# Performance work log

Measured on AMD Instinct MI355X. Metric: run time of the kernel, lower is better.

The kernel has to match this reference:

```python
import jax, jax.numpy as jnp
import numpy as np

B, S, D, H, L = 2, 4096, 768, 12, 2
DH = D // H
W = 256            # one-sided sliding window (longformer-base attention_window=512)
VOCAB = 50265
SEP_ID = 2
N_SEPS = 63
G = N_SEPS + 1     # global tokens: <s> at pos 0 + all </s> separators
FF = 4 * D
C = 7
NEG = -1e9


def layer_norm(x, s, b, eps=1e-5):
    m = x.mean(-1, keepdims=True)
    v = ((x - m) ** 2).mean(-1, keepdims=True)
    return (x - m) * jax.lax.rsqrt(v + eps) * s + b


def setup_inputs():
    key = jax.random.key(0)
    keys = iter(jax.random.split(key, 64))
    def nrm(shape, sd=0.02):
        return jax.random.normal(next(keys), shape, jnp.float32) * sd
    input_ids = jax.random.randint(next(keys), (B, S), 5, VOCAB, dtype=jnp.int32)
    input_ids = input_ids.at[:, 0].set(0)  # <s>
    sep_pos = (jnp.arange(N_SEPS) + 1) * (S // (N_SEPS + 1))  # 64,128,...,4032
    input_ids = input_ids.at[:, sep_pos].set(SEP_ID)
    return dict(
        emb_tok=nrm((VOCAB, D)), emb_pos=nrm((S, D)),
        ln_e_s=jnp.ones((D,)), ln_e_b=jnp.zeros((D,)),
        Wq=nrm((L, D, D)), bq=jnp.zeros((L, D)),
        Wk=nrm((L, D, D)), bk=jnp.zeros((L, D)),
        Wv=nrm((L, D, D)), bv=jnp.zeros((L, D)),
        Wqg=nrm((L, D, D)), bqg=jnp.zeros((L, D)),
        Wkg=nrm((L, D, D)), bkg=jnp.zeros((L, D)),
        Wvg=nrm((L, D, D)), bvg=jnp.zeros((L, D)),
        Wo=nrm((L, D, D)), bo=jnp.zeros((L, D)),
        ln1_s=jnp.ones((L, D)), ln1_b=jnp.zeros((L, D)),
        Wf1=nrm((L, D, FF)), bf1=jnp.zeros((L, FF)),
        Wf2=nrm((L, FF, D)), bf2=jnp.zeros((L, D)),
        ln2_s=jnp.ones((L, D)), ln2_b=jnp.zeros((L, D)),
        Wc=nrm((D, C)), bc=jnp.zeros((C,)),
        input_ids=input_ids,
        attention_mask=jnp.ones((B, S), jnp.int32),
        left_overlap=2, right_overlap=2,
    )


def _forward(emb_tok, emb_pos, ln_e_s, ln_e_b, Wq, bq, Wk, bk, Wv, bv,
             Wqg, bqg, Wkg, bkg, Wvg, bvg, Wo, bo, ln1_s, ln1_b,
             Wf1, bf1, Wf2, bf2, ln2_s, ln2_b, Wc, bc,
             input_ids, attention_mask, left_overlap, right_overlap):
    pos = jnp.arange(S)
    # global attention mask: first token + every </s> token (as in the torch forward)
    g_mask = (input_ids == SEP_ID) | (pos[None, :] == 0)                         # [B,S]
    idx_g = jax.vmap(lambda m: jnp.nonzero(m, size=G, fill_value=0)[0])(g_mask)  # [B,G]
    am = attention_mask.astype(jnp.float32)
    key_local_ok = am * (1.0 - g_mask.astype(jnp.float32))  # globals excluded from windowed keys
    nb = S // W
    band_idx = jnp.arange(nb)[:, None] * W + jnp.arange(3 * W)[None, :]  # [nb,3W] into W-padded seq
    rel = jnp.arange(3 * W)[None, :] - W - jnp.arange(W)[:, None]        # key_pos - query_pos
    band_ok = (jnp.abs(rel) <= W)[None, None, None]                       # [1,1,1,W,3W]
    kv_ok = jnp.pad(key_local_ok, ((0, 0), (W, W)))[:, band_idx] > 0      # [B,nb,3W]
    mask = band_ok & kv_ok[:, None, :, None, :]                           # [B,1,nb,W,3W]
    scale = float(DH) ** -0.5
    bix = jnp.arange(B)[:, None]

    x = emb_tok[input_ids] + emb_pos[None]
    x = layer_norm(x, ln_e_s, ln_e_b)
    for l in range(L):
        q = (x @ Wq[l] + bq[l]).reshape(B, S, H, DH)
        k = (x @ Wk[l] + bk[l]).reshape(B, S, H, DH)
        v = (x @ Wv[l] + bv[l]).reshape(B, S, H, DH)
        kb = jnp.pad(k, ((0, 0), (W, W), (0, 0), (0, 0)))[:, band_idx]    # [B,nb,3W,H,DH]
        vb = jnp.pad(v, ((0, 0), (W, W), (0, 0), (0, 0)))[:, band_idx]
        s_band = jnp.einsum('bnqhd,bnkhd->bhnqk', q.reshape(B, nb, W, H, DH), kb) * scale
        s_band = jnp.where(mask, s_band, NEG)
        kg = jnp.take_along_axis(k, idx_g[:, :, None, None], axis=1)      # [B,G,H,DH]
        vg = jnp.take_along_axis(v, idx_g[:, :, None, None], axis=1)
        s_glob = jnp.einsum('bqhd,bghd->bhqg', q, kg) * scale
        probs = jax.nn.softmax(
            jnp.concatenate([s_band.reshape(B, H, S, 3 * W), s_glob], axis=-1), axis=-1)
        out = (jnp.einsum('bhnqk,bnkhd->bnqhd',
                          probs[..., :3 * W].reshape(B, H, nb, W, 3 * W), vb).reshape(B, S, H, DH)
               + jnp.einsum('bhqg,bghd->bqhd', probs[..., 3 * W:], vg)).reshape(B, S, D)
        # global query rows: full attention over all tokens with dedicated global projections
        xg = jnp.take_along_axis(x, idx_g[:, :, None], axis=1)            # [B,G,D]
        qg = (xg @ Wqg[l] + bqg[l]).reshape(B, G, H, DH)
        kga = (x @ Wkg[l] + bkg[l]).reshape(B, S, H, DH)
        vga = (x @ Wvg[l] + bvg[l]).reshape(B, S, H, DH)
        sg = jnp.where(am[:, None, None, :] > 0,
                       jnp.einsum('bghd,bshd->bhgs', qg, kga) * scale, NEG)
        og = jnp.einsum('bhgs,bshd->bghd', jax.nn.softmax(sg, axis=-1), vga).reshape(B, G, D)
        out = out.at[bix, idx_g].set(og)
        x = layer_norm(x + out @ Wo[l] + bo[l], ln1_s[l], ln1_b[l])
        x = layer_norm(x + jax.nn.gelu(x @ Wf1[l] + bf1[l]) @ Wf2[l] + bf2[l], ln2_s[l], ln2_b[l])
    # classification head (eval-mode dropout = identity). Faithful to the torch code,
    # which gathers hidden states at token POSITION j for j in [left, n_seps - right).
    core = x[:, left_overlap:N_SEPS - right_overlap, :]                    # [B, n_core, D]
    return (core @ Wc + bc).reshape(-1, C)


def reference(emb_tok, emb_pos, ln_e_s, ln_e_b, Wq, bq, Wk, bk, Wv, bv,
              Wqg, bqg, Wkg, bkg, Wvg, bvg, Wo, bo, ln1_s, ln1_b,
              Wf1, bf1, Wf2, bf2, ln2_s, ln2_b, Wc, bc,
              input_ids, attention_mask, left_overlap, right_overlap):
    return _forward(emb_tok, emb_pos, ln_e_s, ln_e_b, Wq, bq, Wk, bk, Wv, bv,
                    Wqg, bqg, Wkg, bkg, Wvg, bvg, Wo, bo, ln1_s, ln1_b,
                    Wf1, bf1, Wf2, bf2, ln2_s, ln2_b, Wc, bc,
                    input_ids, attention_mask, left_overlap, right_overlap)
```

## Files before the change

kernel.cpp:

```cpp
#include <hip/hip_runtime.h>
#include <hip/hip_bf16.h>
#include <stdint.h>

#define B_ 2
#define S_ 4096
#define D_ 768
#define H_ 12
#define DH_ 64
#define L_ 2
#define W_ 256
#define G_ 64
#define FF_ 3072
#define C_ 7
#define SEP_ 2
#define NEG_ (-1000000000.0f)
#define NC_ 16

typedef __attribute__((ext_vector_type(8))) short short8;
typedef __attribute__((ext_vector_type(4))) float f32x4;

__device__ __forceinline__ float bfu2f(unsigned short u) {
    return __uint_as_float(((unsigned int)u) << 16);
}
__device__ __forceinline__ unsigned short f2bfu(float f) {
// ... 172 lines not shown
    int slice = bz;
    int kper = K / gridDim.z;
    int kbeg = slice * kper;
    GEMM256_CORE(A, Wt, K, kbeg, kper);
    float bj[4];
#pragma unroll
    for (int nj = 0; nj < 4; nj++)
        bj[nj] = (slice == 0) ? bias[n0 + (wc << 6) + nj * 16 + l16] : 0.f;
    float* outp = (slice == 0) ? Cf : Cf2;
#pragma unroll
    for (int mi = 0; mi < 8; mi++)
#pragma unroll
        for (int nj = 0; nj < 4; nj++) {
            int col = n0 + (wc << 6) + nj * 16 + l16;
#pragma unroll
            for (int rr = 0; rr < 4; rr++) {
                int row = m0 + (wr << 7) + mi * 16 + quad * 4 + rr;
                float v = acc[mi][nj][rr] + bj[nj];
                if (act) v = gelu_tanh(v);
                if (outp) outp[(size_t)row * N + col] = v;
                else      Cb[(size_t)row * N + col] = f2bfu(v);
            }
        }
}

struct P5 {
    const unsigned short* Wt[5];
    const float* Wf[5];
    const float* bias[5];
    unsigned short* out[5];
};
__global__ __launch_bounds__(512, 1) void k_qkv5_256(
    const unsigned short* __restrict__ A, P5 p) {
    int bx = blockIdx.x, by = blockIdx.y, bz = blockIdx.z;
    xcd_remap(bx, by, bz);
    const unsigned short* __restrict__ Wt = p.Wt[bz];
    const float* __restrict__ bias = p.bias[bz];
    unsigned short* __restrict__ Cb = p.out[bz];
    const int K = D_;
    int m0 = by << 8, n0 = bx << 8;
    GEMM256_CORE(A, Wt, K, 0, K);
    float bj[4];
#pragma unroll
    for (int nj = 0; nj < 4; nj++) bj[nj] = bias[n0 + (wc << 6) + nj * 16 + l16];
#pragma unroll
    for (int mi = 0; mi < 8; mi++)
#pragma unroll
        for (int nj = 0; nj < 4; nj++) {
            int col = n0 + (wc << 6) + nj * 16 + l16;
#pragma unroll
            for (int rr = 0; rr < 4; rr++) {
                int row = m0 + (wr << 7) + mi * 16 + quad * 4 + rr;
                float v = acc[mi][nj][rr] + bj[nj];
                size_t adr = ((((size_t)(row >> 12)) * H_ + (col >> 6)) * S_ +
                              (row & (S_ - 1))) * DH_ + (col & 63);
                Cb[adr] = f2bfu(v);
            }
        }
}

#define GEMM_COMPUTE(Ab, Bb)                                                             \
    {                                                                                    \
        short8 af[4], bf[4];                                                             \
        _Pragma("unroll")                                                                \
        for (int i_ = 0; i_ < 4; i_++)                                                   \
            af[i_] = *(const short8*)&(Ab)[(wm + i_ * 16 + l16) * 32 + quad * 8];        \
        _Pragma("unroll")                                                                \
        for (int j_ = 0; j_ < 4; j_++)                                                   \
            bf[j_] = *(const short8*)&(Bb)[(wn + j_ * 16 + l16) * 32 + quad * 8];        \
        _Pragma("unroll")                                                                \
        for (int i_ = 0; i_ < 4; i_++)                                                   \
            _Pragma("unroll")                                                            \
            for (int j_ = 0; j_ < 4; j_++)                                               \
                acc[i_][j_] = __builtin_amdgcn_mfma_f32_16x16x32_bf16(af[i_], bf[j_],    \
                                                                      acc[i_][j_], 0, 0, 0); \
    }

#define WAIT_VM0_BARRIER()                                   \
    {                                                        \
        asm volatile("s_waitcnt vmcnt(0)" ::: "memory");     \
        __builtin_amdgcn_s_barrier();                        \
    }

__global__ __launch_bounds__(256) void k_wtrans(
    const float* __restrict__ src, unsigned short* __restrict__ dst,
    int K, int N, size_t dstStride) {
    int l = blockIdx.z;
    src += (size_t)l * K * N;
    dst += (size_t)l * dstStride;
    __shared__ unsigned short tile[32][36];
    int t = threadIdx.x;
    int r = t >> 3, c4 = (t & 7) << 2;
    int k0 = blockIdx.y << 5, n0 = blockIdx.x << 5;
    float4 v = *(const float4*)(src + (size_t)(k0 + r) * N + n0 + c4);
    tile[c4 + 0][r] = f2bfu(v.x);
    tile[c4 + 1][r] = f2bfu(v.y);
    tile[c4 + 2][r] = f2bfu(v.z);
    tile[c4 + 3][r] = f2bfu(v.w);
    __syncthreads();
    ushort4 o;
    o.x = tile[r][c4 + 0]; o.y = tile[r][c4 + 1];
    o.z = tile[r][c4 + 2]; o.w = tile[r][c4 + 3];
    *(ushort4*)(dst + (size_t)(n0 + r) * K + k0 + c4) = o;
}

__global__ __launch_bounds__(256) void k_embed_ln(
    const int* __restrict__ ids, const float* __restrict__ etok,
    const float* __restrict__ epos, const float* __restrict__ lns,
    const float* __restrict__ lnb, float* __restrict__ x,
    unsigned short* __restrict__ xb) {
    int row = (blockIdx.x << 2) + (threadIdx.x >> 6);
    int lane = threadIdx.x & 63;
    int s = row & (S_ - 1);
    int id = ids[row];
    const float4* ep = (const float4*)(etok + (size_t)id * D_);
    const float4* pp = (const float4*)(epos + (size_t)s * D_);
    float4 a[3];
    float sum = 0.f, sum2 = 0.f;
#pragma unroll
    for (int i = 0; i < 3; i++) {
        float4 ev = ep[lane + i * 64];
        float4 pv = pp[lane + i * 64];
        ev.x += pv.x; ev.y += pv.y; ev.z += pv.z; ev.w += pv.w;
        a[i] = ev;
        sum  += ev.x + ev.y + ev.z + ev.w;
        sum2 += ev.x * ev.x + ev.y * ev.y + ev.z * ev.z + ev.w * ev.w;
    }
#pragma unroll
    for (int off = 1; off < 64; off <<= 1) {
        sum += __shfl_xor(sum, off);
        sum2 += __shfl_xor(sum2, off);
    }
    float mean = sum * (1.0f / D_);
    float var = sum2 * (1.0f / D_) - mean * mean;
    float rs = rsqrtf(var + 1e-5f);
    float4* xp = (float4*)(x + (size_t)row * D_);
#pragma unroll
    for (int i = 0; i < 3; i++) {
        float4 g = *(const float4*)(lns + lane * 4 + i * 256);
        float4 bb = *(const float4*)(lnb + lane * 4 + i * 256);
        float4 v;
        v.x = (a[i].x - mean) * rs * g.x + bb.x;
        v.y = (a[i].y - mean) * rs * g.y + bb.y;
        v.z = (a[i].z - mean) * rs * g.z + bb.z;
        v.w = (a[i].w - mean) * rs * g.w + bb.w;
        xp[lane + i * 64] = v;
        ushort4 u; u.x = f2bfu(v.x); u.y = f2bfu(v.y); u.z = f2bfu(v.z); u.w = f2bfu(v.w);
        *(ushort4*)(xb + (size_t)row * D_ + lane * 4 + i * 256) = u;
    }
}

__global__ __launch_bounds__(256) void k_add_ln(
    float* __restrict__ x, const float* __restrict__ y, const float* __restrict__ y2,
    const float* __restrict__ lns, const float* __restrict__ lnb,
    unsigned short* __restrict__ xb) {
    int row = (blockIdx.x << 2) + (threadIdx.x >> 6);
    int lane = threadIdx.x & 63;
    float4* xp = (float4*)(x + (size_t)row * D_);
    const float4* yp = (const float4*)(y + (size_t)row * D_);
    const float4* y2p = y2 ? (const float4*)(y2 + (size_t)row * D_) : nullptr;
    float4 a[3];
    float sum = 0.f, sum2 = 0.f;
#pragma unroll
    for (int i = 0; i < 3; i++) {
        float4 xv = xp[lane + i * 64];
        float4 yv = yp[lane + i * 64];
        xv.x += yv.x; xv.y += yv.y; xv.z += yv.z; xv.w += yv.w;
        if (y2p) {
            float4 zv = y2p[lane + i * 64];
            xv.x += zv.x; xv.y += zv.y; xv.z += zv.z; xv.w += zv.w;
        }
        a[i] = xv;
        sum  += xv.x + xv.y + xv.z + xv.w;
        sum2 += xv.x * xv.x + xv.y * xv.y + xv.z * xv.z + xv.w * xv.w;
    }
#pragma unroll
// ... 146 lines not shown
    unsigned short* __restrict__ Cb = p.out[bz];
    const int N = D_, K = D_;
    int t = threadIdx.x;
    int wave = t >> 6, lane = t & 63, l16 = lane & 15, quad = lane >> 4;
    int m0 = by << 7, n0 = bx << 7;
    int wm = (wave >> 1) << 6, wn = (wave & 1) << 6;
    f32x4 acc[4][4];
#pragma unroll
    for (int i = 0; i < 4; i++)
#pragma unroll
        for (int j = 0; j < 4; j++) acc[i][j] = (f32x4){0.f, 0.f, 0.f, 0.f};

    int ch = wave * 128 + lane;
    int srow = ch >> 2, spos = ch & 3;
    const unsigned short* ag = A + (size_t)(m0 + srow) * K + spos * 8;

    if (Wt) {
        const unsigned short* bg = Wt + (size_t)(n0 + srow) * K + spos * 8;
        gl16(ag, As + wave * 1024);
        gl16(ag + (size_t)16 * K, As + wave * 1024 + 512);
        gl16(bg, Bs + wave * 1024);
        gl16(bg + (size_t)16 * K, Bs + wave * 1024 + 512);
        WAIT_VM0_BARRIER();
        int cur = 0;
        for (int k0 = 0; k0 < K; k0 += 32) {
            int koff = k0 + 32;
            if (koff < K) {
                int nb = cur ^ 1;
                gl16(ag + koff, As + nb * 4096 + wave * 1024);
                gl16(ag + koff + (size_t)16 * K, As + nb * 4096 + wave * 1024 + 512);
                gl16(bg + koff, Bs + nb * 4096 + wave * 1024);
                gl16(bg + koff + (size_t)16 * K, Bs + nb * 4096 + wave * 1024 + 512);
            }
            const unsigned short* Ab = As + cur * 4096;
            const unsigned short* Bb = Bs + cur * 4096;
            GEMM_COMPUTE(Ab, Bb);
            WAIT_VM0_BARRIER();
            cur ^= 1;
        }
    } else {
        int bn = t & 127, bkh = (t >> 7) << 4;
        for (int k0 = 0; k0 < K; k0 += 32) {
            gl16(ag + k0, As + wave * 1024);
            gl16(ag + k0 + (size_t)16 * K, As + wave * 1024 + 512);
            const float* bp = Wf + (size_t)(k0 + bkh) * N + n0 + bn;
            unsigned int pk[8];
#pragma unroll
            for (int i = 0; i < 8; i++) {
                unsigned int lo = f2bfu(bp[(size_t)(2 * i) * N]);
                unsigned int hi = f2bfu(bp[(size_t)(2 * i + 1) * N]);
                pk[i] = lo | (hi << 16);
            }
            *(uint4*)&Bs[bn * 32 + bkh] = *(uint4*)&pk[0];
            *(uint4*)&Bs[bn * 32 + bkh + 8] = *(uint4*)&pk[4];
            __syncthreads();
            GEMM_COMPUTE(As, Bs);
            __syncthreads();
        }
    }
    float bj[4];
#pragma unroll
    for (int j = 0; j < 4; j++) bj[j] = bias[n0 + wn + j * 16 + l16];
#pragma unroll
    for (int i = 0; i < 4; i++)
#pragma unroll
        for (int j = 0; j < 4; j++) {
            int col = n0 + wn + j * 16 + l16;
#pragma unroll
            for (int r = 0; r < 4; r++) {
                int row = m0 + wm + i * 16 + quad * 4 + r;
                float v = acc[i][j][r] + bj[j];
                size_t adr = ((((size_t)(row >> 12)) * H_ + (col >> 6)) * S_ +
                              (row & (S_ - 1))) * DH_ + (col & 63);
                Cb[adr] = f2bfu(v);
            }
        }
}

__global__ __launch_bounds__(256) void k_lattn(
    const unsigned short* __restrict__ q, const unsigned short* __restrict__ k,
    const unsigned short* __restrict__ v, const int* __restrict__ ids,
    const int* __restrict__ am, const int* __restrict__ idxg,
    unsigned short* __restrict__ Tb) {
    int s0 = blockIdx.x << 6, h = blockIdx.y, b = blockIdx.z;
    int t = threadIdx.x;
    int wave = t >> 6, lane = t & 63, l16 = lane & 15, quad = lane >> 4;

    __shared__ unsigned short Ks[2][64][72];
    __shared__ unsigned short Vt[2][64][72];
    __shared__ unsigned short Ps[64][72];
    __shared__ unsigned char keyok[2][64];

    const size_t headbase = (((size_t)b * H_) + h) * S_;
    int qrow = s0 + wave * 16 + l16;
    const unsigned short* qptr = q + (headbase + qrow) * DH_;
    short8 qa0 = *(const short8*)(qptr + quad * 8);
    short8 qa1 = *(const short8*)(qptr + 32 + quad * 8);

    f32x4 O[4];
#pragma unroll
    for (int nf = 0; nf < 4; nf++) O[nf] = (f32x4){0.f, 0.f, 0.f, 0.f};
    float m_run[4] = {-3.4e38f, -3.4e38f, -3.4e38f, -3.4e38f};
    float l_run[4] = {0.f, 0.f, 0.f, 0.f};

    int kbase = s0 - 256;
    int sr = t >> 2, sc = t & 3;

    uint4 k0v, k1v, v0v, v1v; bool okf = false;

    auto FETCH = [&](int tile) {
        int sK, sclamp;
        if (tile < 9) {
            sK = kbase + tile * 64 + sr;
            bool inr = (sK >= 0) && (sK < S_);
            sclamp = inr ? sK : 0;
            okf = inr && (am[b * S_ + sclamp] != 0) &&
                  !((ids[b * S_ + sclamp] == SEP_) || (sK == 0));
        } else {
            sclamp = idxg[b * G_ + sr];
            okf = true;
        }
        const unsigned short* srcK = k + (headbase + sclamp) * DH_;
        const unsigned short* srcV = v + (headbase + sclamp) * DH_;
        k0v = *(const uint4*)(srcK + sc * 8);
        k1v = *(const uint4*)(srcK + (sc + 4) * 8);
        v0v = *(const uint4*)(srcV + sc * 8);
        v1v = *(const uint4*)(srcV + (sc + 4) * 8);
    };
    auto WRITE = [&](int buf) {
        if (sc == 0) keyok[buf][sr] = okf ? 1 : 0;
        *(uint4*)&Ks[buf][sr][sc * 8] = k0v;
        *(uint4*)&Ks[buf][sr][(sc + 4) * 8] = k1v;
        STAGE_V_SWZ(Vt[buf], v0v, v1v, sr, sc);
    };

    FETCH(0); WRITE(0);
    __syncthreads();

    for (int tile = 0; tile < 10; tile++) {
        int cur = tile & 1;
        if (tile < 9) FETCH(tile + 1);

        f32x4 Sf[4];
#pragma unroll
        for (int nf = 0; nf < 4; nf++) {
            short8 b0 = *(const short8*)&Ks[cur][nf * 16 + l16][quad * 8];
            short8 b1 = *(const short8*)&Ks[cur][nf * 16 + l16][32 + quad * 8];
            f32x4 a = (f32x4){0.f, 0.f, 0.f, 0.f};
            a = __builtin_amdgcn_mfma_f32_16x16x32_bf16(qa0, b0, a, 0, 0, 0);
            a = __builtin_amdgcn_mfma_f32_16x16x32_bf16(qa1, b1, a, 0, 0, 0);
            Sf[nf] = a;
        }
        int ktb = kbase + tile * 64;
        bool kval[4];
#pragma unroll
        for (int nf = 0; nf < 4; nf++)
            kval[nf] = (tile == 9) || (keyok[cur][nf * 16 + l16] != 0);
        float P_[4][4];
        float mt[4];
#pragma unroll
        for (int r = 0; r < 4; r++) {
            int qs = s0 + wave * 16 + quad * 4 + r;
            float mx = -3.4e38f;
#pragma unroll
            for (int nf = 0; nf < 4; nf++) {
                int ks2 = ktb + nf * 16 + l16;
                bool ok = kval[nf] && ((tile == 9) || (ks2 >= qs - 256 && ks2 <= qs + 256));
                float sv = ok ? Sf[nf][r] * 0.125f : NEG_;
                P_[nf][r] = sv;
                mx = fmaxf(mx, sv);
            }
            mt[r] = mx;
        }
#pragma unroll
        for (int off = 1; off < 16; off <<= 1)
#pragma unroll
            for (int r = 0; r < 4; r++) mt[r] = fmaxf(mt[r], __shfl_xor(mt[r], off));
        float alpha[4], lt[4];
#pragma unroll
        for (int r = 0; r < 4; r++) {
            float mn = fmaxf(m_run[r], mt[r]);
            alpha[r] = __expf(m_run[r] - mn);
            m_run[r] = mn; lt[r] = 0.f;
        }
#pragma unroll
        for (int nf = 0; nf < 4; nf++)
#pragma unroll
            for (int r = 0; r < 4; r++) {
                float p = (P_[nf][r] > -1.0e8f) ? __expf(P_[nf][r] - m_run[r]) : 0.f;
                P_[nf][r] = p; lt[r] += p;
            }
#pragma unroll
        for (int off = 1; off < 16; off <<= 1)
#pragma unroll
            for (int r = 0; r < 4; r++) lt[r] += __shfl_xor(lt[r], off);
#pragma unroll
        for (int r = 0; r < 4; r++) l_run[r] = l_run[r] * alpha[r] + lt[r];
#pragma unroll
        for (int nf = 0; nf < 4; nf++) {
            O[nf][0] *= alpha[0]; O[nf][1] *= alpha[1];
            O[nf][2] *= alpha[2]; O[nf][3] *= alpha[3];
        }
#pragma unroll
        for (int nf = 0; nf < 4; nf++)
#pragma unroll
            for (int r = 0; r < 4; r++)
                Ps[wave * 16 + quad * 4 + r][nf * 16 + l16] = f2bfu(P_[nf][r]);
#pragma unroll
        for (int hh = 0; hh < 2; hh++) {
            short8 pa = *(const short8*)&Ps[wave * 16 + l16][hh * 32 + quad * 8];
#pragma unroll
            for (int nf = 0; nf < 4; nf++) {
                short8 vb8 = READ_V_SWZ(Vt[cur], nf * 16 + l16, hh);
                O[nf] = __builtin_amdgcn_mfma_f32_16x16x32_bf16(pa, vb8, O[nf], 0, 0, 0);
            }
        }
        if (tile < 9) WRITE(cur ^ 1);
        __syncthreads();
    }
#pragma unroll
    for (int r = 0; r < 4; r++) {
        int qs = s0 + wave * 16 + quad * 4 + r;
        float invl = 1.0f / l_run[r];
        size_t base = ((size_t)(b * S_ + qs)) * D_ + h * DH_;
#pragma unroll
        for (int nf = 0; nf < 4; nf++)
            Tb[base + nf * 16 + l16] = f2bfu(O[nf][r] * invl);
    }
}

__global__ __launch_bounds__(256) void k_gattn_part(
    const unsigned short* __restrict__ qg, const unsigned short* __restrict__ kga,
    const unsigned short* __restrict__ vga, const int* __restrict__ am,
    float* __restrict__ Opart, float* __restrict__ mbuf, float* __restrict__ lbuf) {
    int c = blockIdx.x, h = blockIdx.y, b = blockIdx.z;
    int t = threadIdx.x;
    int wave = t >> 6, lane = t & 63, l16 = lane & 15, quad = lane >> 4;

    __shared__ unsigned short Ks[2][64][72];
    __shared__ unsigned short Vt[2][64][72];
    __shared__ unsigned short Ps[64][72];
    __shared__ unsigned char keyok[2][64];

    const size_t headbase = (((size_t)b * H_) + h) * S_;
    int grow = wave * 16 + l16;
    const unsigned short* qptr = qg + ((size_t)(b * G_ + grow)) * D_ + h * DH_;
    short8 qa0 = *(const short8*)(qptr + quad * 8);
    short8 qa1 = *(const short8*)(qptr + 32 + quad * 8);

    f32x4 O[4];
#pragma unroll
    for (int nf = 0; nf < 4; nf++) O[nf] = (f32x4){0.f, 0.f, 0.f, 0.f};
    float m_run[4] = {-3.4e38f, -3.4e38f, -3.4e38f, -3.4e38f};
    float l_run[4] = {0.f, 0.f, 0.f, 0.f};

    int kbase = c * 256;
    int sr = t >> 2, sc = t & 3;

    uint4 k0v, k1v, v0v, v1v; bool okf = false;

    auto FETCH = [&](int tile) {
        int sK = kbase + tile * 64 + sr;
        okf = (am[b * S_ + sK] != 0);
        const unsigned short* srcK = kga + (headbase + sK) * DH_;
        const unsigned short* srcV = vga + (headbase + sK) * DH_;
        k0v = *(const uint4*)(srcK + sc * 8);
        k1v = *(const uint4*)(srcK + (sc + 4) * 8);
        v0v = *(const uint4*)(srcV + sc * 8);
        v1v = *(const uint4*)(srcV + (sc + 4) * 8);
    };
    auto WRITE = [&](int buf) {
        if (sc == 0) keyok[buf][sr] = okf ? 1 : 0;
        *(uint4*)&Ks[buf][sr][sc * 8] = k0v;
        *(uint4*)&Ks[buf][sr][(sc + 4) * 8] = k1v;
        STAGE_V_SWZ(Vt[buf], v0v, v1v, sr, sc);
    };

    FETCH(0); WRITE(0);
    __syncthreads();

    for (int tile = 0; tile < 4; tile++) {
        int cur = tile & 1;
        if (tile < 3) FETCH(tile + 1);

        f32x4 Sf[4];
#pragma unroll
        for (int nf = 0; nf < 4; nf++) {
            short8 b0 = *(const short8*)&Ks[cur][nf * 16 + l16][quad * 8];
            short8 b1 = *(const short8*)&Ks[cur][nf * 16 + l16][32 + quad * 8];
            f32x4 a = (f32x4){0.f, 0.f, 0.f, 0.f};
            a = __builtin_amdgcn_mfma_f32_16x16x32_bf16(qa0, b0, a, 0, 0, 0);
            a = __builtin_amdgcn_mfma_f32_16x16x32_bf16(qa1, b1, a, 0, 0, 0);
            Sf[nf] = a;
        }
        bool kval[4];
#pragma unroll
        for (int nf = 0; nf < 4; nf++) kval[nf] = (keyok[cur][nf * 16 + l16] != 0);
        float P_[4][4];
        float mt[4];
#pragma unroll
        for (int r = 0; r < 4; r++) {
            float mx = -3.4e38f;
#pragma unroll
            for (int nf = 0; nf < 4; nf++) {
                float sv = kval[nf] ? Sf[nf][r] * 0.125f : NEG_;
                P_[nf][r] = sv;
                mx = fmaxf(mx, sv);
            }
            mt[r] = mx;
        }
#pragma unroll
// ... 4 lines not shown
#pragma unroll
        for (int r = 0; r < 4; r++) {
            float mn = fmaxf(m_run[r], mt[r]);
            alpha[r] = __expf(m_run[r] - mn);
            m_run[r] = mn; lt[r] = 0.f;
        }
#pragma unroll
        for (int nf = 0; nf < 4; nf++)
#pragma unroll
            for (int r = 0; r < 4; r++) {
                float p = (P_[nf][r] > -1.0e8f) ? __expf(P_[nf][r] - m_run[r]) : 0.f;
                P_[nf][r] = p; lt[r] += p;
            }
#pragma unroll
        for (int off = 1; off < 16; off <<= 1)
#pragma unroll
            for (int r = 0; r < 4; r++) lt[r] += __shfl_xor(lt[r], off);
#pragma unroll
        for (int r = 0; r < 4; r++) l_run[r] = l_run[r] * alpha[r] + lt[r];
#pragma unroll
        for (int nf = 0; nf < 4; nf++) {
            O[nf][0] *= alpha[0]; O[nf][1] *= alpha[1];
            O[nf][2] *= alpha[2]; O[nf][3] *= alpha[3];
        }
#pragma unroll
        for (int nf = 0; nf < 4; nf++)
#pragma unroll
            for (int r = 0; r < 4; r++)
                Ps[wave * 16 + quad * 4 + r][nf * 16 + l16] = f2bfu(P_[nf][r]);
#pragma unroll
        for (int hh = 0; hh < 2; hh++) {
            short8 pa = *(const short8*)&Ps[wave * 16 + l16][hh * 32 + quad * 8];
#pragma unroll
            for (int nf = 0; nf < 4; nf++) {
                short8 vb8 = READ_V_SWZ(Vt[cur], nf * 16 + l16, hh);
                O[nf] = __builtin_amdgcn_mfma_f32_16x16x32_bf16(pa, vb8, O[nf], 0, 0, 0);
            }
        }
        if (tile < 3) WRITE(cur ^ 1);
        __syncthreads();
    }
    size_t bhc = ((size_t)(b * H_ + h)) * NC_ + c;
#pragma unroll
    for (int r = 0; r < 4; r++) {
        int row = wave * 16 + quad * 4 + r;
#pragma unroll
        for (int nf = 0; nf < 4; nf++)
            Opart[bhc * (G_ * DH_) + (size_t)row * DH_ + nf * 16 + l16] = O[nf][r];
        if (l16 == 0) {
            mbuf[bhc * G_ + row] = m_run[r];
            lbuf[bhc * G_ + row] = l_run[r];
        }
    }
}

__global__ __launch_bounds__(64) void k_gattn_comb(
    const float* __restrict__ Opart, const float* __restrict__ mbuf,
    const float* __restrict__ lbuf, const int* __restrict__ idxg,
    unsigned short* __restrict__ Tb) {
    int g = blockIdx.x, h = blockIdx.y, b = blockIdx.z;
    int d = threadIdx.x;
    size_t bh = (size_t)(b * H_ + h);
    float M = -3.4e38f;
    float mv[NC_];
#pragma unroll
    for (int c = 0; c < NC_; c++) {
        mv[c] = mbuf[(bh * NC_ + c) * G_ + g];
        M = fmaxf(M, mv[c]);
    }
    float L = 0.f, o = 0.f;
#pragma unroll
    for (int c = 0; c < NC_; c++) {
        float e = __expf(mv[c] - M);
        L += lbuf[(bh * NC_ + c) * G_ + g] * e;
        o += Opart[(bh * NC_ + c) * (G_ * DH_) + (size_t)g * DH_ + d] * e;
    }
    int srow = idxg[b * G_ + g];
    Tb[((size_t)(b * S_ + srow)) * D_ + h * DH_ + d] = f2bfu(o / L);
}

__global__ __launch_bounds__(256) void k_gemm(
    const float* __restrict__ A, const float* __restrict__ Bw,
    const float* __restrict__ bias, float* __restrict__ Cf,
    unsigned short* __restrict__ Cb, int M, int N, int K, int act) {
    __shared__ float As[16][68];
    __shared__ float Bs[16][68];
    int tl = threadIdx.x;
    int tx = tl & 15, ty = tl >> 4;
    int m0 = blockIdx.y << 6, n0 = blockIdx.x << 6;
    float c[4][4] = {{0.f}};
    int arow = tl >> 2, akk = (tl & 3) << 2;
    int bkk = tl >> 4, bcol = (tl & 15) << 2;
    for (int k0 = 0; k0 < K; k0 += 16) {
        float4 a4 = *(const float4*)(A + (size_t)(m0 + arow) * K + k0 + akk);
        As[akk + 0][arow] = a4.x; As[akk + 1][arow] = a4.y;
        As[akk + 2][arow] = a4.z; As[akk + 3][arow] = a4.w;
        float4 b4 = *(const float4*)(Bw + (size_t)(k0 + bkk) * N + n0 + bcol);
        Bs[bkk][bcol + 0] = b4.x; Bs[bkk][bcol + 1] = b4.y;
        Bs[bkk][bcol + 2] = b4.z; Bs[bkk][bcol + 3] = b4.w;
        __syncthreads();
#pragma unroll
        for (int kk = 0; kk < 16; kk++) {
            float4 av = *(const float4*)&As[kk][ty << 2];
            float4 bv = *(const float4*)&Bs[kk][tx << 2];
            float aa[4] = {av.x, av.y, av.z, av.w};
            float bb[4] = {bv.x, bv.y, bv.z, bv.w};
#pragma unroll
            for (int i = 0; i < 4; i++)
#pragma unroll
                for (int j = 0; j < 4; j++) c[i][j] += aa[i] * bb[j];
        }
        __syncthreads();
    }
    float bias4[4];
#pragma unroll
    for (int j = 0; j < 4; j++) bias4[j] = bias[n0 + (tx << 2) + j];
#pragma unroll
    for (int i = 0; i < 4; i++) {
        int mrow = m0 + (ty << 2) + i;
        float v0 = c[i][0] + bias4[0], v1 = c[i][1] + bias4[1];
        float v2 = c[i][2] + bias4[2], v3 = c[i][3] + bias4[3];
        if (act) { v0 = gelu_tanh(v0); v1 = gelu_tanh(v1); v2 = gelu_tanh(v2); v3 = gelu_tanh(v3); }
        if (Cf) {
            float4 o; o.x = v0; o.y = v1; o.z = v2; o.w = v3;
            *(float4*)(Cf + (size_t)mrow * N + n0 + (tx << 2)) = o;
        } else {
            ushort4 o; o.x = f2bfu(v0); o.y = f2bfu(v1); o.z = f2bfu(v2); o.w = f2bfu(v3);
            *(ushort4*)(Cb + (size_t)mrow * N + n0 + (tx << 2)) = o;
        }
    }
}

__global__ __launch_bounds__(256) void k_gather_xg(
    const float* __restrict__ x, const int* __restrict__ idxg, float* __restrict__ xg) {
    int bg = blockIdx.x;
    int b = bg / G_;
    int srow = idxg[bg];
    for (int d = threadIdx.x; d < D_; d += 256)
        xg[(size_t)bg * D_ + d] = x[((size_t)(b * S_ + srow)) * D_ + d];
}

__global__ __launch_bounds__(256) void k_classifier(
    const float* __restrict__ x, const float* __restrict__ Wc,
    const float* __restrict__ bc, const int* __restrict__ lo_p,
    int rows_pb, float* __restrict__ out) {
    int r = blockIdx.x;
    int b = r / rows_pb, i = r % rows_pb;
    int s = lo_p[0] + i;
    int t = threadIdx.x;
    __shared__ float xr[D_];
    __shared__ float red[256];
    const float* xrow = x + ((size_t)(b * S_ + s)) * D_;
    for (int d = t; d < D_; d += 256) xr[d] = xrow[d];
    __syncthreads();
    for (int c = 0; c < C_; c++) {
        float loc = 0.f;
        for (int d = t; d < D_; d += 256) loc += xr[d] * Wc[d * C_ + c];
        red[t] = loc; __syncthreads();
        for (int o = 128; o; o >>= 1) { if (t < o) red[t] += red[t + o]; __syncthreads(); }
        if (t == 0) out[r * C_ + c] = red[0] + bc[c];
        __syncthreads();
    }
}

extern "C" void kernel_launch(void* const* d_in, const int* in_sizes, int n_in,
                              void* d_out, int out_size, void* d_ws, size_t ws_size,
                              hipStream_t stream) {
    (void)in_sizes; (void)n_in;
    const float* emb_tok = (const float*)d_in[0];
    const float* emb_pos = (const float*)d_in[1];
    const float* ln_e_s = (const float*)d_in[2];
    const float* ln_e_b = (const float*)d_in[3];
    const float* Wq  = (const float*)d_in[4];
    const float* bq  = (const float*)d_in[5];
    const float* Wk  = (const float*)d_in[6];
    const float* bk  = (const float*)d_in[7];
    const float* Wv  = (const float*)d_in[8];
    const float* bv  = (const float*)d_in[9];
    const float* Wqg = (const float*)d_in[10];
    const float* bqg = (const float*)d_in[11];
    const float* Wkg = (const float*)d_in[12];
    const float* bkg = (const float*)d_in[13];
    const float* Wvg = (const float*)d_in[14];
    const float* bvg = (const float*)d_in[15];
    const float* Wo  = (const float*)d_in[16];
    const float* bo  = (const float*)d_in[17];
    const float* ln1_s = (const float*)d_in[18];
    const float* ln1_b = (const float*)d_in[19];
    const float* Wf1 = (const float*)d_in[20];
    const float* bf1 = (const float*)d_in[21];
    const float* Wf2 = (const float*)d_in[22];
    const float* bf2 = (const float*)d_in[23];
    const float* ln2_s = (const float*)d_in[24];
    const float* ln2_b = (const float*)d_in[25];
    const float* Wc  = (const float*)d_in[26];
    const float* bc  = (const float*)d_in[27];
    const int* input_ids = (const int*)d_in[28];
    const int* attn_mask = (const int*)d_in[29];
    const int* lo        = (const int*)d_in[30];

    const size_t SZB = (size_t)B_ * S_ * D_;
    const size_t D2 = (size_t)D_ * D_;
    const size_t PL = 6 * D2 + 2 * (size_t)D_ * FF_;
    uint8_t* w = (uint8_t*)d_ws;
    float*          x    = (float*)w;
    unsigned short* xb   = (unsigned short*)(w + 4 * SZB);
    float*          P    = (float*)(w + 6 * SZB);
    unsigned short* qb   = (unsigned short*)(w + 10 * SZB);
    unsigned short* kb   = (unsigned short*)(w + 12 * SZB);
    unsigned short* vb   = (unsigned short*)(w + 14 * SZB);
    unsigned short* kgab = (unsigned short*)(w + 16 * SZB);
    unsigned short* vgab = (unsigned short*)(w + 18 * SZB);
    unsigned short* Hb   = (unsigned short*)(w + 10 * SZB);
    unsigned short* Tb   = (unsigned short*)(w + 20 * SZB);
    float* xg = (float*)(w + 22 * SZB);
    unsigned short* qgb = (unsigned short*)(w + 22 * SZB + (size_t)B_ * G_ * D_ * 4);
    int* idxg = (int*)(w + 22 * SZB + (size_t)B_ * G_ * D_ * 4 + (size_t)B_ * G_ * D_ * 2);
    float* Opart = (float*)(w + 23 * SZB);
    float* mbuf  = (float*)(w + 24 * SZB);
    float* lbuf  = mbuf + (size_t)B_ * H_ * NC_ * G_;

    const size_t P2_OFF = 24 * SZB + (1u << 20);
    const size_t WB_OFF = P2_OFF + 4 * SZB;
    const size_t NEED_P2 = WB_OFF;
    const size_t NEED_W = WB_OFF + L_ * PL * 2;
    float* P2 = (float*)(w + P2_OFF);
    unsigned short* wb = (unsigned short*)(w + WB_OFF);
    const int useW = (ws_size >= NEED_W) ? 1 : 0;
    const int useSplit = (ws_size >= NEED_P2) ? 1 : 0;

    const int BS = B_ * S_;

    if (useW) {
        k_wtrans<<<dim3(D_/32, D_/32, L_), 256, 0, stream>>>(Wq,  wb + 0*D2, D_, D_, PL);
        k_wtrans<<<dim3(D_/32, D_/32, L_), 256, 0, stream>>>(Wk,  wb + 1*D2, D_, D_, PL);
        k_wtrans<<<dim3(D_/32, D_/32, L_), 256, 0, stream>>>(Wv,  wb + 2*D2, D_, D_, PL);
        k_wtrans<<<dim3(D_/32, D_/32, L_), 256, 0, stream>>>(Wkg, wb + 3*D2, D_, D_, PL);
        k_wtrans<<<dim3(D_/32, D_/32, L_), 256, 0, stream>>>(Wvg, wb + 4*D2, D_, D_, PL);
        k_wtrans<<<dim3(D_/32, D_/32, L_), 256, 0, stream>>>(Wo,  wb + 5*D2, D_, D_, PL);
        k_wtrans<<<dim3(FF_/32, D_/32, L_), 256, 0, stream>>>(Wf1, wb + 6*D2, D_, FF_, PL);
        k_wtrans<<<dim3(D_/32, FF_/32, L_), 256, 0, stream>>>(Wf2, wb + 6*D2 + (size_t)D_*FF_, FF_, D_, PL);
    }

    k_embed_ln<<<BS / 4, 256, 0, stream>>>(input_ids, emb_tok, emb_pos, ln_e_s, ln_e_b, x, xb);
    k_idx<<<B_, 256, 0, stream>>>(input_ids, idxg);

    dim3 g_ds(D_ / 128, BS / 128, useSplit ? 2 : 1);
    dim3 g_d5(D_ / 128, BS / 128, 5);
    dim3 g_ff(FF_ / 128, BS / 128);
    dim3 g_qg(D_ / 64, (B_ * G_) / 64);

    for (int l = 0; l < L_; l++) {
        const unsigned short* wbl = wb + (size_t)l * PL;
        P5 p5;
        p5.Wf[0] = Wq  + (size_t)l * D2;  p5.bias[0] = bq  + l * D_;  p5.out[0] = qb;
        p5.Wf[1] = Wk  + (size_t)l * D2;  p5.bias[1] = bk  + l * D_;  p5.out[1] = kb;
        p5.Wf[2] = Wv  + (size_t)l * D2;  p5.bias[2] = bv  + l * D_;  p5.out[2] = vb;
        p5.Wf[3] = Wkg + (size_t)l * D2;  p5.bias[3] = bkg + l * D_;  p5.out[3] = kgab;
        p5.Wf[4] = Wvg + (size_t)l * D2;  p5.bias[4] = bvg + l * D_;  p5.out[4] = vgab;
        for (int i = 0; i < 5; i++) p5.Wt[i] = useW ? (wbl + (size_t)i * D2) : nullptr;
        const float* Wqg_l = Wqg + (size_t)l * D2;
        const float* Wo_l  = Wo  + (size_t)l * D2;
        const float* Wf1_l = Wf1 + (size_t)l * D_ * FF_;
        const float* Wf2_l = Wf2 + (size_t)l * FF_ * D_;
        const unsigned short* Wo_t  = useW ? (wbl + 5 * D2) : nullptr;
        const unsigned short* Wf1_t = useW ? (wbl + 6 * D2) : nullptr;
        const unsigned short* Wf2_t = useW ? (wbl + 6 * D2 + (size_t)D_ * FF_) : nullptr;

        if (useW) {
            k_qkv5_256<<<dim3(D_ / 256, BS / 256, 5), 512, 0, stream>>>(xb, p5);
        } else {
            k_gemm_qkv5<<<g_d5, 256, 0, stream>>>(xb, p5);
        }
        k_lattn<<<dim3(S_ / 64, H_, B_), 256, 0, stream>>>(qb, kb, vb, input_ids, attn_mask, idxg, Tb);
        k_gather_xg<<<B_ * G_, 256, 0, stream>>>(x, idxg, xg);
        k_gemm<<<g_qg, 256, 0, stream>>>(xg, Wqg_l, bqg + l * D_, nullptr, qgb, B_ * G_, D_, D_, 0);
        k_gattn_part<<<dim3(NC_, H_, B_), 256, 0, stream>>>(qgb, kgab, vgab, attn_mask, Opart, mbuf, lbuf);
        k_gattn_comb<<<dim3(G_, H_, B_), 64, 0, stream>>>(Opart, mbuf, lbuf, idxg, Tb);
        if (useW) {
            k_gemm256_nt<<<dim3(D_ / 256, BS / 256, useSplit ? 2 : 1), 512, 0, stream>>>(
                Tb, Wo_t, bo + l * D_, P, P2, nullptr, BS, D_, D_, 0);
            k_add_ln<<<BS / 4, 256, 0, stream>>>(x, P, useSplit ? P2 : nullptr, ln1_s + l * D_, ln1_b + l * D_, xb);
            k_gemm256_nt<<<dim3(FF_ / 256, BS / 256, 1), 512, 0, stream>>>(
                xb, Wf1_t, bf1 + l * FF_, nullptr, nullptr, Hb, BS, FF_, D_, 1);
            k_gemm256_nt<<<dim3(D_ / 256, BS / 256, useSplit ? 2 : 1), 512, 0, stream>>>(
                Hb, Wf2_t, bf2 + l * D_, P, P2, nullptr, BS, D_, FF_, 0);
            k_add_ln<<<BS / 4, 256, 0, stream>>>(x, P, useSplit ? P2 : nullptr, ln2_s + l * D_, ln2_b + l * D_, xb);
        } else {
            k_gemm_mfma<<<g_ds, 256, 0, stream>>>(Tb, Wo_t, Wo_l, bo + l * D_, P, P2, nullptr, BS, D_, D_, 0);
            k_add_ln<<<BS / 4, 256, 0, stream>>>(x, P, useSplit ? P2 : nullptr, ln1_s + l * D_, ln1_b + l * D_, xb);
            k_gemm_mfma<<<g_ff, 256, 0, stream>>>(xb, Wf1_t, Wf1_l, bf1 + l * FF_, nullptr, nullptr, Hb, BS, FF_, D_, 1);
            k_gemm_mfma<<<g_ds, 256, 0, stream>>>(Hb, Wf2_t, Wf2_l, bf2 + l * D_, P, P2, nullptr, BS, D_, FF_, 0);
            k_add_ln<<<BS / 4, 256, 0, stream>>>(x, P, useSplit ? P2 : nullptr, ln2_s + l * D_, ln2_b + l * D_, xb);
        }
    }

    int rows = out_size / C_;
    int rows_pb = rows / B_;
    k_classifier<<<rows, 256, 0, stream>>>(x, Wc, bc, lo, rows_pb, (float*)d_out);
}
```

Baseline: 1.070 ms.

## Double query rows per local-attention block, merge weight transposes, fuse global gather

The local attention kernel now handles 128 query rows per block, with each wave covering two 16-row slices. This reuses every staged K/V tile across twice as many queries, costs 11 instead of 10 key tiles per block, and remaps block indices so neighbouring blocks land on the same XCD. The eight weight-transpose launches are merged into one kernel that dispatches on a cumulative block table. The global-token gather is folded into the Qg GEMM's A-row pointer, dropping a launch and an intermediate buffer. The trade-offs are higher register pressure from the doubled accumulators and half as many attention blocks.

```diff
diff --git a/kernel.cpp b/kernel.cpp
--- a/kernel.cpp
+++ b/kernel.cpp
@@ -278,16 +278,29 @@
         __builtin_amdgcn_s_barrier();                        \
     }
 
-__global__ __launch_bounds__(256) void k_wtrans(
-    const float* __restrict__ src, unsigned short* __restrict__ dst,
-    int K, int N, size_t dstStride) {
-    int l = blockIdx.z;
-    src += (size_t)l * K * N;
-    dst += (size_t)l * dstStride;
+struct WT8 {
+    const float* src[8];
+    unsigned short* dst[8];
+    int K[8], N[8];
+    int cum[9];
+};
+__global__ __launch_bounds__(256) void k_wtrans_all(WT8 p, size_t PLs) {
+    int blk = blockIdx.x;
+    int op = 0;
+#pragma unroll
+    for (int i = 0; i < 7; i++) op += (blk >= p.cum[i + 1]) ? 1 : 0;
+    int local = blk - p.cum[op];
+    int K = p.K[op], N = p.N[op];
+    int nx = N >> 5, ny = K >> 5;
+    int l = local / (nx * ny);
+    int rem = local - l * (nx * ny);
+    int bxx = rem % nx, byy = rem / nx;
+    const float* src = p.src[op] + (size_t)l * K * N;
+    unsigned short* dst = p.dst[op] + (size_t)l * PLs;
     __shared__ unsigned short tile[32][36];
     int t = threadIdx.x;
     int r = t >> 3, c4 = (t & 7) << 2;
-    int k0 = blockIdx.y << 5, n0 = blockIdx.x << 5;
+    int k0 = byy << 5, n0 = bxx << 5;
     float4 v = *(const float4*)(src + (size_t)(k0 + r) * N + n0 + c4);
     tile[c4 + 0][r] = f2bfu(v.x);
     tile[c4 + 1][r] = f2bfu(v.y);
@@ -600,7 +613,12 @@
     const unsigned short* __restrict__ v, const int* __restrict__ ids,
     const int* __restrict__ am, const int* __restrict__ idxg,
     unsigned short* __restrict__ Tb) {
-    int s0 = blockIdx.x << 6, h = blockIdx.y, b = blockIdx.z;
+    int flat = blockIdx.x + 32 * (blockIdx.y + H_ * blockIdx.z);
+    int xcd = flat & 7, idx = flat >> 3;
+    int i4 = idx & 3, hb = idx >> 2;
+    int bx = (xcd << 2) + i4;
+    int h = hb % H_, b = hb / H_;
+    int s0 = bx << 7;
     int t = threadIdx.x;
     int wave = t >> 6, lane = t & 63, l16 = lane & 15, quad = lane >> 4;
 
@@ -610,25 +628,32 @@
     __shared__ unsigned char keyok[2][64];
 
     const size_t headbase = (((size_t)b * H_) + h) * S_;
-    int qrow = s0 + wave * 16 + l16;
-    const unsigned short* qptr = q + (headbase + qrow) * DH_;
-    short8 qa0 = *(const short8*)(qptr + quad * 8);
-    short8 qa1 = *(const short8*)(qptr + 32 + quad * 8);
-
-    f32x4 O[4];
-#pragma unroll
-    for (int nf = 0; nf < 4; nf++) O[nf] = (f32x4){0.f, 0.f, 0.f, 0.f};
-    float m_run[4] = {-3.4e38f, -3.4e38f, -3.4e38f, -3.4e38f};
-    float l_run[4] = {0.f, 0.f, 0.f, 0.f};
+    short8 qa[2][2];
+#pragma unroll
+    for (int qs = 0; qs < 2; qs++) {
+        int qrow = s0 + wave * 32 + qs * 16 + l16;
+        const unsigned short* qptr = q + (headbase + qrow) * DH_;
+        qa[qs][0] = *(const short8*)(qptr + quad * 8);
+        qa[qs][1] = *(const short8*)(qptr + 32 + quad * 8);
+    }
+
+    f32x4 O[2][4];
+    float m_run[2][4], l_run[2][4];
+#pragma unroll
+    for (int qs = 0; qs < 2; qs++)
+#pragma unroll
+        for (int nf = 0; nf < 4; nf++) {
+            O[qs][nf] = (f32x4){0.f, 0.f, 0.f, 0.f};
+            m_run[qs][nf] = -3.4e38f; l_run[qs][nf] = 0.f;
+        }
 
     int kbase = s0 - 256;
     int sr = t >> 2, sc = t & 3;
-
     uint4 k0v, k1v, v0v, v1v; bool okf = false;
 
     auto FETCH = [&](int tile) {
         int sK, sclamp;
-        if (tile < 9) {
+        if (tile < 10) {
             sK = kbase + tile * 64 + sr;
             bool inr = (sK >= 0) && (sK < S_);
             sclamp = inr ? sK : 0;
@@ -655,96 +680,102 @@
     FETCH(0); WRITE(0);
     __syncthreads();
 
-    for (int tile = 0; tile < 10; tile++) {
+    for (int tile = 0; tile < 11; tile++) {
         int cur = tile & 1;
-        if (tile < 9) FETCH(tile + 1);
-
-        f32x4 Sf[4];
-#pragma unroll
-        for (int nf = 0; nf < 4; nf++) {
-            short8 b0 = *(const short8*)&Ks[cur][nf * 16 + l16][quad * 8];
-            short8 b1 = *(const short8*)&Ks[cur][nf * 16 + l16][32 + quad * 8];
-            f32x4 a = (f32x4){0.f, 0.f, 0.f, 0.f};
-            a = __builtin_amdgcn_mfma_f32_16x16x32_bf16(qa0, b0, a, 0, 0, 0);
-            a = __builtin_amdgcn_mfma_f32_16x16x32_bf16(qa1, b1, a, 0, 0, 0);
-            Sf[nf] = a;
-        }
+        if (tile < 10) FETCH(tile + 1);
+
         int ktb = kbase + tile * 64;
         bool kval[4];
 #pragma unroll
         for (int nf = 0; nf < 4; nf++)
-            kval[nf] = (tile == 9) || (keyok[cur][nf * 16 + l16] != 0);
-        float P_[4][4];
-        float mt[4];
+            kval[nf] = (tile == 10) || (keyok[cur][nf * 16 + l16] != 0);
+
+#pragma unroll
+        for (int qs = 0; qs < 2; qs++) {
+            f32x4 Sf[4];
+#pragma unroll
+            for (int nf = 0; nf < 4; nf++) {
+                short8 b0 = *(const short8*)&Ks[cur][nf * 16 + l16][quad * 8];
+                short8 b1 = *(const short8*)&Ks[cur][nf * 16 + l16][32 + quad * 8];
+                f32x4 a = (f32x4){0.f, 0.f, 0.f, 0.f};
+                a = __builtin_amdgcn_mfma_f32_16x16x32_bf16(qa[qs][0], b0, a, 0, 0, 0);
+                a = __builtin_amdgcn_mfma_f32_16x16x32_bf16(qa[qs][1], b1, a, 0, 0, 0);
+                Sf[nf] = a;
+            }
+            float P_[4][4];
+            float mt[4];
+#pragma unroll
+            for (int r = 0; r < 4; r++) {
+                int qrc = s0 + wave * 32 + qs * 16 + quad * 4 + r;
+                float mx = -3.4e38f;
+#pragma unroll
+                for (int nf = 0; nf < 4; nf++) {
+                    int ks2 = ktb + nf * 16 + l16;
+                    bool ok = kval[nf] && ((tile == 10) || (ks2 >= qrc - 256 && ks2 <= qrc + 256));
+                    float sv = ok ? Sf[nf][r] * 0.125f : NEG_;
+                    P_[nf][r] = sv;
+                    mx = fmaxf(mx, sv);
+                }
+                mt[r] = mx;
+            }
+#pragma unroll
+            for (int off = 1; off < 16; off <<= 1)
+#pragma unroll
+                for (int r = 0; r < 4; r++) mt[r] = fmaxf(mt[r], __shfl_xor(mt[r], off));
+            float alpha[4], lt[4];
+#pragma unroll
+            for (int r = 0; r < 4; r++) {
+                float mn = fmaxf(m_run[qs][r], mt[r]);
+                alpha[r] = __expf(m_run[qs][r] - mn);
+                m_run[qs][r] = mn; lt[r] = 0.f;
+            }
+#pragma unroll
+            for (int nf = 0; nf < 4; nf++)
+#pragma unroll
+                for (int r = 0; r < 4; r++) {
+                    float p = (P_[nf][r] > -1.0e8f) ? __expf(P_[nf][r] - m_run[qs][r]) : 0.f;
+                    P_[nf][r] = p; lt[r] += p;
+                }
+#pragma unroll
+            for (int off = 1; off < 16; off <<= 1)
+#pragma unroll
+                for (int r = 0; r < 4; r++) lt[r] += __shfl_xor(lt[r], off);
+#pragma unroll
+            for (int r = 0; r < 4; r++) l_run[qs][r] = l_run[qs][r] * alpha[r] + lt[r];
+#pragma unroll
+            for (int nf = 0; nf < 4; nf++) {
+                O[qs][nf][0] *= alpha[0]; O[qs][nf][1] *= alpha[1];
+                O[qs][nf][2] *= alpha[2]; O[qs][nf][3] *= alpha[3];
+            }
+#pragma unroll
+            for (int nf = 0; nf < 4; nf++)
+#pragma unroll
+                for (int r = 0; r < 4; r++)
+                    Ps[wave * 16 + quad * 4 + r][nf * 16 + l16] = f2bfu(P_[nf][r]);
+#pragma unroll
+            for (int hh = 0; hh < 2; hh++) {
+                short8 pa = *(const short8*)&Ps[wave * 16 + l16][hh * 32 + quad * 8];
+#pragma unroll
+                for (int nf = 0; nf < 4; nf++) {
+                    short8 vb8 = READ_V_SWZ(Vt[cur], nf * 16 + l16, hh);
+                    O[qs][nf] = __builtin_amdgcn_mfma_f32_16x16x32_bf16(pa, vb8, O[qs][nf], 0, 0, 0);
+                }
+            }
+        }
+        if (tile < 10) WRITE(cur ^ 1);
+        __syncthreads();
+    }
+#pragma unroll
+    for (int qs = 0; qs < 2; qs++)
 #pragma unroll
         for (int r = 0; r < 4; r++) {
-            int qs = s0 + wave * 16 + quad * 4 + r;
-            float mx = -3.4e38f;
-#pragma unroll
-            for (int nf = 0; nf < 4; nf++) {
-                int ks2 = ktb + nf * 16 + l16;
-                bool ok = kval[nf] && ((tile == 9) || (ks2 >= qs - 256 && ks2 <= qs + 256));
-                float sv = ok ? Sf[nf][r] * 0.125f : NEG_;
-                P_[nf][r] = sv;
-                mx = fmaxf(mx, sv);
-            }
-            mt[r] = mx;
-        }
-#pragma unroll
-        for (int off = 1; off < 16; off <<= 1)
-#pragma unroll
-            for (int r = 0; r < 4; r++) mt[r] = fmaxf(mt[r], __shfl_xor(mt[r], off));
-        float alpha[4], lt[4];
-#pragma unroll
-        for (int r = 0; r < 4; r++) {
-            float mn = fmaxf(m_run[r], mt[r]);
-            alpha[r] = __expf(m_run[r] - mn);
-            m_run[r] = mn; lt[r] = 0.f;
-        }
-#pragma unroll
-        for (int nf = 0; nf < 4; nf++)
-#pragma unroll
-            for (int r = 0; r < 4; r++) {
-                float p = (P_[nf][r] > -1.0e8f) ? __expf(P_[nf][r] - m_run[r]) : 0.f;
-                P_[nf][r] = p; lt[r] += p;
-            }
-#pragma unroll
-        for (int off = 1; off < 16; off <<= 1)
-#pragma unroll
-            for (int r = 0; r < 4; r++) lt[r] += __shfl_xor(lt[r], off);
-#pragma unroll
-        for (int r = 0; r < 4; r++) l_run[r] = l_run[r] * alpha[r] + lt[r];
-#pragma unroll
-        for (int nf = 0; nf < 4; nf++) {
-            O[nf][0] *= alpha[0]; O[nf][1] *= alpha[1];
-            O[nf][2] *= alpha[2]; O[nf][3] *= alpha[3];
-        }
-#pragma unroll
-        for (int nf = 0; nf < 4; nf++)
-#pragma unroll
-            for (int r = 0; r < 4; r++)
-                Ps[wave * 16 + quad * 4 + r][nf * 16 + l16] = f2bfu(P_[nf][r]);
-#pragma unroll
-        for (int hh = 0; hh < 2; hh++) {
-            short8 pa = *(const short8*)&Ps[wave * 16 + l16][hh * 32 + quad * 8];
-#pragma unroll
-            for (int nf = 0; nf < 4; nf++) {
-                short8 vb8 = READ_V_SWZ(Vt[cur], nf * 16 + l16, hh);
-                O[nf] = __builtin_amdgcn_mfma_f32_16x16x32_bf16(pa, vb8, O[nf], 0, 0, 0);
-            }
-        }
-        if (tile < 9) WRITE(cur ^ 1);
-        __syncthreads();
-    }
-#pragma unroll
-    for (int r = 0; r < 4; r++) {
-        int qs = s0 + wave * 16 + quad * 4 + r;
-        float invl = 1.0f / l_run[r];
-        size_t base = ((size_t)(b * S_ + qs)) * D_ + h * DH_;
-#pragma unroll
-        for (int nf = 0; nf < 4; nf++)
-            Tb[base + nf * 16 + l16] = f2bfu(O[nf][r] * invl);
-    }
+            int qrow = s0 + wave * 32 + qs * 16 + quad * 4 + r;
+            float invl = 1.0f / l_run[qs][r];
+            size_t base = ((size_t)(b * S_ + qrow)) * D_ + h * DH_;
+#pragma unroll
+            for (int nf = 0; nf < 4; nf++)
+                Tb[base + nf * 16 + l16] = f2bfu(O[qs][nf][r] * invl);
+        }
 }
 
 __global__ __launch_bounds__(256) void k_gattn_part(
@@ -915,7 +946,8 @@
 __global__ __launch_bounds__(256) void k_gemm(
     const float* __restrict__ A, const float* __restrict__ Bw,
     const float* __restrict__ bias, float* __restrict__ Cf,
-    unsigned short* __restrict__ Cb, int M, int N, int K, int act) {
+    unsigned short* __restrict__ Cb, int M, int N, int K, int act,
+    const float* __restrict__ xsrc, const int* __restrict__ idxg) {
     __shared__ float As[16][68];
     __shared__ float Bs[16][68];
     int tl = threadIdx.x;
@@ -924,8 +956,17 @@
     float c[4][4] = {{0.f}};
     int arow = tl >> 2, akk = (tl & 3) << 2;
     int bkk = tl >> 4, bcol = (tl & 15) << 2;
+    const float* arow_p;
+    if (idxg) {
+        int bg = m0 + arow;
+        int bb = bg >> 6;
+        int srow = idxg[bg];
+        arow_p = xsrc + ((size_t)(bb * S_ + srow)) * D_;
+    } else {
+        arow_p = A + (size_t)(m0 + arow) * K;
+    }
     for (int k0 = 0; k0 < K; k0 += 16) {
-        float4 a4 = *(const float4*)(A + (size_t)(m0 + arow) * K + k0 + akk);
+        float4 a4 = *(const float4*)(arow_p + k0 + akk);
         As[akk + 0][arow] = a4.x; As[akk + 1][arow] = a4.y;
         As[akk + 2][arow] = a4.z; As[akk + 3][arow] = a4.w;
         float4 b4 = *(const float4*)(Bw + (size_t)(k0 + bkk) * N + n0 + bcol);
@@ -962,15 +1003,6 @@
             *(ushort4*)(Cb + (size_t)mrow * N + n0 + (tx << 2)) = o;
         }
     }
-}
-
-__global__ __launch_bounds__(256) void k_gather_xg(
-    const float* __restrict__ x, const int* __restrict__ idxg, float* __restrict__ xg) {
-    int bg = blockIdx.x;
-    int b = bg / G_;
-    int srow = idxg[bg];
-    for (int d = threadIdx.x; d < D_; d += 256)
-        xg[(size_t)bg * D_ + d] = x[((size_t)(b * S_ + srow)) * D_ + d];
 }
 
 __global__ __launch_bounds__(256) void k_classifier(
@@ -1046,7 +1078,6 @@
     unsigned short* vgab = (unsigned short*)(w + 18 * SZB);
     unsigned short* Hb   = (unsigned short*)(w + 10 * SZB);
     unsigned short* Tb   = (unsigned short*)(w + 20 * SZB);
-    float* xg = (float*)(w + 22 * SZB);
     unsigned short* qgb = (unsigned short*)(w + 22 * SZB + (size_t)B_ * G_ * D_ * 4);
     int* idxg = (int*)(w + 22 * SZB + (size_t)B_ * G_ * D_ * 4 + (size_t)B_ * G_ * D_ * 2);
     float* Opart = (float*)(w + 23 * SZB);
@@ -1065,14 +1096,22 @@
     const int BS = B_ * S_;
 
     if (useW) {
-        k_wtrans<<<dim3(D_/32, D_/32, L_), 256, 0, stream>>>(Wq,  wb + 0*D2, D_, D_, PL);
-        k_wtrans<<<dim3(D_/32, D_/32, L_), 256, 0, stream>>>(Wk,  wb + 1*D2, D_, D_, PL);
-        k_wtrans<<<dim3(D_/32, D_/32, L_), 256, 0, stream>>>(Wv,  wb + 2*D2, D_, D_, PL);
-        k_wtrans<<<dim3(D_/32, D_/32, L_), 256, 0, stream>>>(Wkg, wb + 3*D2, D_, D_, PL);
-        k_wtrans<<<dim3(D_/32, D_/32, L_), 256, 0, stream>>>(Wvg, wb + 4*D2, D_, D_, PL);
-        k_wtrans<<<dim3(D_/32, D_/32, L_), 256, 0, stream>>>(Wo,  wb + 5*D2, D_, D_, PL);
-        k_wtrans<<<dim3(FF_/32, D_/32, L_), 256, 0, stream>>>(Wf1, wb + 6*D2, D_, FF_, PL);
-        k_wtrans<<<dim3(D_/32, FF_/32, L_), 256, 0, stream>>>(Wf2, wb + 6*D2 + (size_t)D_*FF_, FF_, D_, PL);
+        WT8 wt;
+        int cum = 0;
+        auto addop = [&](int opi, const float* s, unsigned short* d, int K, int N) {
+            wt.src[opi] = s; wt.dst[opi] = d; wt.K[opi] = K; wt.N[opi] = N;
+            wt.cum[opi] = cum; cum += L_ * (N / 32) * (K / 32);
+        };
+        addop(0, Wq,  wb + 0 * D2, D_, D_);
+        addop(1, Wk,  wb + 1 * D2, D_, D_);
+        addop(2, Wv,  wb + 2 * D2, D_, D_);
+        addop(3, Wkg, wb + 3 * D2, D_, D_);
+        addop(4, Wvg, wb + 4 * D2, D_, D_);
+        addop(5, Wo,  wb + 5 * D2, D_, D_);
+        addop(6, Wf1, wb + 6 * D2, D_, FF_);
+        addop(7, Wf2, wb + 6 * D2 + (size_t)D_ * FF_, FF_, D_);
+        wt.cum[8] = cum;
+        k_wtrans_all<<<cum, 256, 0, stream>>>(wt, PL);
     }
 
     k_embed_ln<<<BS / 4, 256, 0, stream>>>(input_ids, emb_tok, emb_pos, ln_e_s, ln_e_b, x, xb);
@@ -1105,9 +1144,8 @@
         } else {
             k_gemm_qkv5<<<g_d5, 256, 0, stream>>>(xb, p5);
         }
-        k_lattn<<<dim3(S_ / 64, H_, B_), 256, 0, stream>>>(qb, kb, vb, input_ids, attn_mask, idxg, Tb);
-        k_gather_xg<<<B_ * G_, 256, 0, stream>>>(x, idxg, xg);
-        k_gemm<<<g_qg, 256, 0, stream>>>(xg, Wqg_l, bqg + l * D_, nullptr, qgb, B_ * G_, D_, D_, 0);
+        k_lattn<<<dim3(S_ / 128, H_, B_), 256, 0, stream>>>(qb, kb, vb, input_ids, attn_mask, idxg, Tb);
+        k_gemm<<<g_qg, 256, 0, stream>>>(nullptr, Wqg_l, bqg + l * D_, nullptr, qgb, B_ * G_, D_, D_, 0, x, idxg);
         k_gattn_part<<<dim3(NC_, H_, B_), 256, 0, stream>>>(qgb, kgab, vgab, attn_mask, Opart, mbuf, lbuf);
         k_gattn_comb<<<dim3(G_, H_, B_), 64, 0, stream>>>(Opart, mbuf, lbuf, idxg, Tb);
         if (useW) {
```

Result: slower. 1.131 ms (+5.7%).
